# Optimization experiments

Measured on AMD Instinct MI355X. Metric: run time of the kernel, lower is better.

The kernel has to match this reference:

```python
import jax, jax.numpy as jnp
import numpy as np

H_OUT = 8
W_OUT = 8
MAXG = 4  # max adaptive sampling grid per bin: ceil((H-1)/H_OUT) with H=32


def _flip_table():
    h, w = H_OUT, W_OUT
    ys = np.repeat(np.arange(h), w)
    xs = np.tile(np.arange(w), h)
    rys = np.repeat(np.arange(h - 1, -1, -1), w)
    # NOTE: original torch code does arange(w-1,-1,-1).reshape(h,1).repeat(1,w)
    # which makes reverse_xs a per-ROW reversal (requires h==w); replicated faithfully.
    rxs = np.repeat(np.arange(w - 1, -1, -1), w)
    i00 = ys * w + xs
    i01 = ys * w + rxs
    i10 = rys * w + xs
    i11 = rys * w + rxs
    # original stacks [i00, i01, i01, i10, i11]; idx_idxs in {0..3} so entry for
    # (y_rev=1,x_rev=0) is i01 (duplicated) and (1,1) hits i10; i11 is unused. Replicated.
    return jnp.asarray(np.stack([i00, i01, i01, i10, i11]), dtype=jnp.int32)

_TABLE = _flip_table()


def _axis_samples(start, bin_sz, grid, n_out, size):
    # start, bin_sz: [N] float; grid: [N] int (adaptive samples per bin along this axis)
    # returns low/high neighbor indices and corner weights, each [N, n_out*MAXG]
    N = start.shape[0]
    g_safe = jnp.maximum(grid, 1).astype(start.dtype)
    ph = jnp.arange(n_out, dtype=start.dtype)
    i = jnp.arange(MAXG, dtype=start.dtype)
    pos = (start[:, None, None]
           + ph[None, :, None] * bin_sz[:, None, None]
           + (i[None, None, :] + 0.5) * (bin_sz / g_safe)[:, None, None])  # [N,n_out,MAXG]
    valid = ((pos >= -1.0) & (pos <= size)
             & (jnp.arange(MAXG)[None, None, :] < grid[:, None, None]))
    p = jnp.clip(pos, 0.0, size - 1)
    low = jnp.floor(p).astype(jnp.int32)
    high = jnp.minimum(low + 1, size - 1)
    l = p - low.astype(p.dtype)
    vf = valid.astype(start.dtype)
    return (low.reshape(N, -1), high.reshape(N, -1),
            ((1.0 - l) * vf).reshape(N, -1), (l * vf).reshape(N, -1))


def _roi_align_flip(feats, batch_idxs, starts, goals):
    B, C, H, W = feats.shape
    N = starts.shape[0]
    s = starts.astype(feats.dtype)
    g = goals.astype(feats.dtype)
    y_min = jnp.minimum(s[:, 0], g[:, 0]); y_max = jnp.maximum(s[:, 0], g[:, 0])
    x_min = jnp.minimum(s[:, 1], g[:, 1]); x_max = jnp.maximum(s[:, 1], g[:, 1])
    y_rev = s[:, 0] > g[:, 0]
    x_rev = s[:, 1] > g[:, 1]
    # torchvision roi_align: aligned=True, spatial_scale=1.0, sampling_ratio=-1
    start_h = y_min - 0.5; start_w = x_min - 0.5
    roi_h = y_max - y_min; roi_w = x_max - x_min
    bin_h = roi_h / H_OUT; bin_w = roi_w / W_OUT
    gh = jnp.ceil(bin_h).astype(jnp.int32)
    gw = jnp.ceil(bin_w).astype(jnp.int32)
    count = jnp.maximum(gh * gw, 1).astype(feats.dtype)
    ylo, yhi, wy0, wy1 = _axis_samples(start_h, bin_h, gh, H_OUT, H)  # [N, H_OUT*MAXG]
    xlo, xhi, wx0, wx1 = _axis_samples(start_w, bin_w, gw, W_OUT, W)  # [N, W_OUT*MAXG]
    fv = feats.reshape(B, C, H * W)[batch_idxs]  # [N,C,H*W] per-box feature slab
    hM, wM = H_OUT * MAXG, W_OUT * MAXG

    def gath(yi, xi):
        lin = (yi[:, :, None] * W + xi[:, None, :]).reshape(N, 1, hM * wM)
        v = jnp.take_along_axis(fv, jnp.broadcast_to(lin, (N, C, hM * wM)), axis=2)
        return v.reshape(N, C, hM, wM)

    def outer(a, b):
        return a[:, None, :, None] * b[:, None, None, :]

    acc = (gath(ylo, xlo) * outer(wy0, wx0)
           + gath(ylo, xhi) * outer(wy0, wx1)
           + gath(yhi, xlo) * outer(wy1, wx0)
           + gath(yhi, xhi) * outer(wy1, wx1))  # [N,C,hM,wM]
    rois = acc.reshape(N, C, H_OUT, MAXG, W_OUT, MAXG).sum(axis=(3, 5))
    rois = rois / count[:, None, None, None]
    # per-box orientation flip via index-table gather
    idx_idxs = y_rev.astype(jnp.int32) * 2 + x_rev.astype(jnp.int32)
    sel = _TABLE[idx_idxs]  # [N, h*w]
    rflat = rois.reshape(N, C, H_OUT * W_OUT)
    out = jnp.take_along_axis(rflat, jnp.broadcast_to(sel[:, None, :], rflat.shape), axis=2)
    return out.reshape(N, C, H_OUT, W_OUT)


def setup_inputs() -> dict:
    key = jax.random.key(0)
    k1, k2, k3, k4 = jax.random.split(key, 4)
    B, C, H, W = 8, 64, 32, 32
    N = 1024  # B * A with A = 128 agents
    feats = jax.random.normal(k1, (B, C, H, W), dtype=jnp.float32)
    batch_idxs = jax.random.randint(k2, (N,), 0, B, dtype=jnp.int32)
    starts = jax.random.randint(k3, (N, 2), 0, H, dtype=jnp.int32)
    goals = jax.random.randint(k4, (N, 2), 0, H, dtype=jnp.int32)
    return {"feats": feats, "batch_idxs": batch_idxs, "starts": starts, "goals": goals}


def reference(feats, batch_idxs, starts, goals):
    return _roi_align_flip(feats, batch_idxs, starts, goals)
```

## Files before the change

kernel.cpp:

```cpp
#include <hip/hip_runtime.h>

#define H_OUT 8
#define W_OUT 8
#define MAXG 4
#define CCHUNK 16
#define RSLOTS 6
#define TSTRIDE 160

__global__ __launch_bounds__(256) void build_tables(
    const int* __restrict__ batch_idxs,
    const int* __restrict__ starts,
    const int* __restrict__ goals,
    float*     __restrict__ tab, int N)
{
    const int t = blockIdx.x * 256 + threadIdx.x;
    if (t >= N * 16) return;
    const int n    = t >> 4;
    const int slot = t & 15;
    const int axis = slot >> 3;
    const int ph   = slot & 7;

    const float s0 = (float)starts[2 * n + 0];
    const float s1 = (float)starts[2 * n + 1];
    const float g0 = (float)goals[2 * n + 0];
    const float g1 = (float)goals[2 * n + 1];
    const float y_min = fminf(s0, g0), y_max = fmaxf(s0, g0);
    const float x_min = fminf(s1, g1), x_max = fmaxf(s1, g1);
    const float bin_h = (y_max - y_min) * 0.125f;
    const float bin_w = (x_max - x_min) * 0.125f;
    const int   gh = (int)ceilf(bin_h);
    const int   gw = (int)ceilf(bin_w);

    const float start = axis ? (x_min - 0.5f) : (y_min - 0.5f);
    const float bin   = axis ? bin_w : bin_h;
    const int   grid  = axis ? gw : gh;
    const float gsafe = (float)(grid > 1 ? grid : 1);

    float wloc[RSLOTS] = {0.f, 0.f, 0.f, 0.f, 0.f, 0.f};
    int base = 0, last = -1;
    for (int i = 0; i < grid; ++i) {
        const float pos = start + (float)ph * bin + ((float)i + 0.5f) * (bin / gsafe);
        const float vf  = (pos >= -1.0f && pos <= 32.0f) ? 1.0f : 0.0f;
        const float p   = fminf(fmaxf(pos, 0.0f), 31.0f);
        const int   lo  = (int)floorf(p);
        const int   hi  = min(lo + 1, 31);
        const float l   = p - (float)lo;
        if (i == 0) base = lo;
        wloc[lo - base] += (1.0f - l) * vf;
        wloc[hi - base] += l * vf;
        last = hi;
    }

    float* __restrict__ rec = tab + (size_t)n * TSTRIDE + axis * 64 + ph * 8;
    #pragma unroll
    for (int k = 0; k < RSLOTS; ++k) rec[k] = wloc[k];
    rec[6] = (float)base;
    rec[7] = (float)((grid > 0) ? (last - base + 1) : 0);
    if (slot == 0) {
        float* __restrict__ tb = tab + (size_t)n * TSTRIDE;
        const bool y_rev = s0 > g0;
        const bool x_rev = s1 > g1;
        tb[128] = 1.0f / fmaxf((float)(gh * gw), 1.0f);
        tb[129] = (float)((y_rev ? 2 : 0) + (x_rev ? 1 : 0));
        tb[130] = (float)batch_idxs[n];
        tb[131] = 0.0f;
    }
}

__global__ __launch_bounds__(256) void roi_main(
    const float* __restrict__ feats,
    const float* __restrict__ tab,
    float*       __restrict__ out,
    int C, int CG)
{
    const int bx  = blockIdx.x;
    const int n   = bx / CG;
    const int cg  = bx - n * CG;
    const int tid = threadIdx.x;

    const float* __restrict__ tb = tab + (size_t)n * TSTRIDE;

    __shared__ float s_t[CCHUNK][H_OUT][36];

    const int py = tid >> 5;
    const int cp = (tid >> 3) & 3;
    const int xq = tid & 7;
    const float4 ya   = *reinterpret_cast<const float4*>(tb + py * 8);
    const float4 yb   = *reinterpret_cast<const float4*>(tb + py * 8 + 4);
    const float4 meta = *reinterpret_cast<const float4*>(tb + 128);

    {
        const int rb = (int)yb.z;
        const int rc = (int)yb.w;
        const int b  = (int)meta.z;
        const float wy[6] = {ya.x, ya.y, ya.z, ya.w, yb.x, yb.y};

        const float* __restrict__ fb =
            feats + ((size_t)b * C + (size_t)(cg * CCHUNK + cp * 4)) * 1024 + xq * 4;

        float4 a0 = {0.f,0.f,0.f,0.f}, a1 = {0.f,0.f,0.f,0.f};
        float4 a2 = {0.f,0.f,0.f,0.f}, a3 = {0.f,0.f,0.f,0.f};
        #pragma unroll
        for (int j = 0; j < 5; ++j) {
            if (j < rc) {
                const float w  = wy[j];
                const int   ro = (rb + j) * 32;
                const float4 r0 = *reinterpret_cast<const float4*>(fb + ro);
                const float4 r1 = *reinterpret_cast<const float4*>(fb + 1024 + ro);
                const float4 r2 = *reinterpret_cast<const float4*>(fb + 2048 + ro);
                const float4 r3 = *reinterpret_cast<const float4*>(fb + 3072 + ro);
                a0.x = fmaf(w, r0.x, a0.x); a0.y = fmaf(w, r0.y, a0.y);
                a0.z = fmaf(w, r0.z, a0.z); a0.w = fmaf(w, r0.w, a0.w);
                a1.x = fmaf(w, r1.x, a1.x); a1.y = fmaf(w, r1.y, a1.y);
                a1.z = fmaf(w, r1.z, a1.z); a1.w = fmaf(w, r1.w, a1.w);
                a2.x = fmaf(w, r2.x, a2.x); a2.y = fmaf(w, r2.y, a2.y);
                a2.z = fmaf(w, r2.z, a2.z); a2.w = fmaf(w, r2.w, a2.w);
                a3.x = fmaf(w, r3.x, a3.x); a3.y = fmaf(w, r3.y, a3.y);
                a3.z = fmaf(w, r3.z, a3.z); a3.w = fmaf(w, r3.w, a3.w);
            }
        }
        const int x0 = xq * 4;
        *reinterpret_cast<float4*>(&s_t[cp * 4 + 0][py][x0]) = a0;
        *reinterpret_cast<float4*>(&s_t[cp * 4 + 1][py][x0]) = a1;
        *reinterpret_cast<float4*>(&s_t[cp * 4 + 2][py][x0]) = a2;
        *reinterpret_cast<float4*>(&s_t[cp * 4 + 3][py][x0]) = a3;
    }

    const int yx = tid & 63;
    const int y  = yx >> 3;
    const int xo = yx & 7;
    const int c0 = tid >> 6;

    const int fc = (int)meta.y;
    int py2, px;
    if (fc == 3)      { py2 = H_OUT - 1 - y; px = xo; }
    else if (fc != 0) { py2 = y;             px = W_OUT - 1 - y; }
    else              { py2 = y;             px = xo; }

    const float4 xa  = *reinterpret_cast<const float4*>(tb + 64 + px * 8);
    const float4 xb4 = *reinterpret_cast<const float4*>(tb + 64 + px * 8 + 4);

    __syncthreads();

    const int   xbi = (int)xb4.z;
    const int   xc  = (int)xb4.w;
    const float wx[6] = {xa.x, xa.y, xa.z, xa.w, xb4.x, xb4.y};
    const float inv_count = meta.x;

    float b0 = 0.f, b1 = 0.f, b2 = 0.f, b3 = 0.f;
    #pragma unroll
    for (int j = 0; j < 5; ++j) {
        if (j < xc) {
            const float w = wx[j];
            b0 = fmaf(w, s_t[c0     ][py2][xbi + j], b0);
            b1 = fmaf(w, s_t[c0 +  4][py2][xbi + j], b1);
            b2 = fmaf(w, s_t[c0 +  8][py2][xbi + j], b2);
            b3 = fmaf(w, s_t[c0 + 12][py2][xbi + j], b3);
        }
    }

    float* __restrict__ ob =
        out + ((size_t)n * C + (size_t)cg * CCHUNK) * (H_OUT * W_OUT);
    ob[tid      ] = b0 * inv_count;
    ob[tid + 256] = b1 * inv_count;
    ob[tid + 512] = b2 * inv_count;
    ob[tid + 768] = b3 * inv_count;
}

extern "C" void kernel_launch(void* const* d_in, const int* in_sizes, int n_in,
                              void* d_out, int out_size, void* d_ws, size_t ws_size,
                              hipStream_t stream) {
    const float* feats      = (const float*)d_in[0];
    const int*   batch_idxs = (const int*)d_in[1];
    const int*   starts     = (const int*)d_in[2];
    const int*   goals      = (const int*)d_in[3];
    float*       out        = (float*)d_out;
    float*       tab        = (float*)d_ws;

    const int N  = in_sizes[1];
    const int C  = out_size / (N * H_OUT * W_OUT);
    const int CG = C / CCHUNK;

    const int tb_blocks = (N * 16 + 255) / 256;
    build_tables<<<tb_blocks, 256, 0, stream>>>(batch_idxs, starts, goals, tab, N);
    roi_main<<<N * CG, 256, 0, stream>>>(feats, tab, out, C, CG);
}
```

Measured before the change: 76.63 us.

## Fuse per-box weight-table construction into main ROI kernel via shared memory

Removes the separate build_tables launch and the global workspace table. Each block now computes the per-box interpolation weights for both axes, plus the flip code and batch index, in its first 16 threads, stores them in shared memory, and synchronises before the main gather. This saves one kernel launch and a global round-trip, at the cost of redundant table computation in every channel-group block, a serial prologue executed by 16 threads, and an extra barrier.

```diff
diff --git a/kernel.cpp b/kernel.cpp
--- a/kernel.cpp
+++ b/kernel.cpp
@@ -2,74 +2,13 @@
 
 #define H_OUT 8
 #define W_OUT 8
-#define MAXG 4
 #define CCHUNK 16
-#define RSLOTS 6
-#define TSTRIDE 160
 
-__global__ __launch_bounds__(256) void build_tables(
-    const int* __restrict__ batch_idxs,
-    const int* __restrict__ starts,
-    const int* __restrict__ goals,
-    float*     __restrict__ tab, int N)
-{
-    const int t = blockIdx.x * 256 + threadIdx.x;
-    if (t >= N * 16) return;
-    const int n    = t >> 4;
-    const int slot = t & 15;
-    const int axis = slot >> 3;
-    const int ph   = slot & 7;
-
-    const float s0 = (float)starts[2 * n + 0];
-    const float s1 = (float)starts[2 * n + 1];
-    const float g0 = (float)goals[2 * n + 0];
-    const float g1 = (float)goals[2 * n + 1];
-    const float y_min = fminf(s0, g0), y_max = fmaxf(s0, g0);
-    const float x_min = fminf(s1, g1), x_max = fmaxf(s1, g1);
-    const float bin_h = (y_max - y_min) * 0.125f;
-    const float bin_w = (x_max - x_min) * 0.125f;
-    const int   gh = (int)ceilf(bin_h);
-    const int   gw = (int)ceilf(bin_w);
-
-    const float start = axis ? (x_min - 0.5f) : (y_min - 0.5f);
-    const float bin   = axis ? bin_w : bin_h;
-    const int   grid  = axis ? gw : gh;
-    const float gsafe = (float)(grid > 1 ? grid : 1);
-
-    float wloc[RSLOTS] = {0.f, 0.f, 0.f, 0.f, 0.f, 0.f};
-    int base = 0, last = -1;
-    for (int i = 0; i < grid; ++i) {
-        const float pos = start + (float)ph * bin + ((float)i + 0.5f) * (bin / gsafe);
-        const float vf  = (pos >= -1.0f && pos <= 32.0f) ? 1.0f : 0.0f;
-        const float p   = fminf(fmaxf(pos, 0.0f), 31.0f);
-        const int   lo  = (int)floorf(p);
-        const int   hi  = min(lo + 1, 31);
-        const float l   = p - (float)lo;
-        if (i == 0) base = lo;
-        wloc[lo - base] += (1.0f - l) * vf;
-        wloc[hi - base] += l * vf;
-        last = hi;
-    }
-
-    float* __restrict__ rec = tab + (size_t)n * TSTRIDE + axis * 64 + ph * 8;
-    #pragma unroll
-    for (int k = 0; k < RSLOTS; ++k) rec[k] = wloc[k];
-    rec[6] = (float)base;
-    rec[7] = (float)((grid > 0) ? (last - base + 1) : 0);
-    if (slot == 0) {
-        float* __restrict__ tb = tab + (size_t)n * TSTRIDE;
-        const bool y_rev = s0 > g0;
-        const bool x_rev = s1 > g1;
-        tb[128] = 1.0f / fmaxf((float)(gh * gw), 1.0f);
-        tb[129] = (float)((y_rev ? 2 : 0) + (x_rev ? 1 : 0));
-        tb[130] = (float)batch_idxs[n];
-        tb[131] = 0.0f;
-    }
-}
-
-__global__ __launch_bounds__(256) void roi_main(
+__global__ __launch_bounds__(256) void roi_fused(
     const float* __restrict__ feats,
-    const float* __restrict__ tab,
+    const int*   __restrict__ batch_idxs,
+    const int*   __restrict__ starts,
+    const int*   __restrict__ goals,
     float*       __restrict__ out,
     int C, int CG)
 {
@@ -78,22 +17,68 @@
     const int cg  = bx - n * CG;
     const int tid = threadIdx.x;
 
-    const float* __restrict__ tb = tab + (size_t)n * TSTRIDE;
+    __shared__ float s_rec[2][8][8];
+    __shared__ float s_meta[4];
+    __shared__ float s_t[CCHUNK][H_OUT][36];
 
-    __shared__ float s_t[CCHUNK][H_OUT][36];
+    if (tid < 16) {
+        const int axis = tid >> 3;
+        const int ph   = tid & 7;
+        const float s0 = (float)starts[2 * n + 0];
+        const float s1 = (float)starts[2 * n + 1];
+        const float g0 = (float)goals[2 * n + 0];
+        const float g1 = (float)goals[2 * n + 1];
+        const float y_min = fminf(s0, g0), y_max = fmaxf(s0, g0);
+        const float x_min = fminf(s1, g1), x_max = fmaxf(s1, g1);
+        const float bin_h = (y_max - y_min) * 0.125f;
+        const float bin_w = (x_max - x_min) * 0.125f;
+        const int   gh = (int)ceilf(bin_h);
+        const int   gw = (int)ceilf(bin_w);
+
+        const float start = axis ? (x_min - 0.5f) : (y_min - 0.5f);
+        const float bin   = axis ? bin_w : bin_h;
+        const int   grid  = axis ? gw : gh;
+        const float gsafe = (float)(grid > 1 ? grid : 1);
+
+        float* __restrict__ rec = &s_rec[axis][ph][0];
+        #pragma unroll
+        for (int k = 0; k < 6; ++k) rec[k] = 0.0f;
+
+        int base = 0, last = -1;
+        for (int i = 0; i < grid; ++i) {
+            const float pos = start + (float)ph * bin + ((float)i + 0.5f) * (bin / gsafe);
+            const float vf  = (pos >= -1.0f && pos <= 32.0f) ? 1.0f : 0.0f;
+            const float p   = fminf(fmaxf(pos, 0.0f), 31.0f);
+            const int   lo  = (int)floorf(p);
+            const int   hi  = min(lo + 1, 31);
+            const float l   = p - (float)lo;
+            if (i == 0) base = lo;
+            rec[lo - base] += (1.0f - l) * vf;
+            rec[hi - base] += l * vf;
+            last = hi;
+        }
+        rec[6] = (float)base;
+        rec[7] = (float)((grid > 0) ? (last - base + 1) : 0);
+        if (tid == 0) {
+            s_meta[0] = 1.0f / fmaxf((float)(gh * gw), 1.0f);
+            s_meta[1] = (float)(((s0 > g0) ? 2 : 0) + ((s1 > g1) ? 1 : 0));
+            s_meta[2] = (float)batch_idxs[n];
+        }
+    }
+    __syncthreads();
 
     const int py = tid >> 5;
     const int cp = (tid >> 3) & 3;
     const int xq = tid & 7;
-    const float4 ya   = *reinterpret_cast<const float4*>(tb + py * 8);
-    const float4 yb   = *reinterpret_cast<const float4*>(tb + py * 8 + 4);
-    const float4 meta = *reinterpret_cast<const float4*>(tb + 128);
-
+    const float4 ya = *reinterpret_cast<const float4*>(&s_rec[0][py][0]);
+    const float4 yb = *reinterpret_cast<const float4*>(&s_rec[0][py][4]);
+    const float inv_count = s_meta[0];
+    const int   fcode     = (int)s_meta[1];
+    const int   b         = (int)s_meta[2];
     {
         const int rb = (int)yb.z;
         const int rc = (int)yb.w;
-        const int b  = (int)meta.z;
-        const float wy[6] = {ya.x, ya.y, ya.z, ya.w, yb.x, yb.y};
+        const float wy[5] = {ya.x, ya.y, ya.z, ya.w, yb.x};
 
         const float* __restrict__ fb =
             feats + ((size_t)b * C + (size_t)(cg * CCHUNK + cp * 4)) * 1024 + xq * 4;
@@ -131,21 +116,19 @@
     const int xo = yx & 7;
     const int c0 = tid >> 6;
 
-    const int fc = (int)meta.y;
     int py2, px;
-    if (fc == 3)      { py2 = H_OUT - 1 - y; px = xo; }
-    else if (fc != 0) { py2 = y;             px = W_OUT - 1 - y; }
-    else              { py2 = y;             px = xo; }
+    if (fcode == 3)      { py2 = H_OUT - 1 - y; px = xo; }
+    else if (fcode != 0) { py2 = y;             px = W_OUT - 1 - y; }
+    else                 { py2 = y;             px = xo; }
 
-    const float4 xa  = *reinterpret_cast<const float4*>(tb + 64 + px * 8);
-    const float4 xb4 = *reinterpret_cast<const float4*>(tb + 64 + px * 8 + 4);
+    const float4 xa  = *reinterpret_cast<const float4*>(&s_rec[1][px][0]);
+    const float4 xb4 = *reinterpret_cast<const float4*>(&s_rec[1][px][4]);
 
     __syncthreads();
 
     const int   xbi = (int)xb4.z;
     const int   xc  = (int)xb4.w;
-    const float wx[6] = {xa.x, xa.y, xa.z, xa.w, xb4.x, xb4.y};
-    const float inv_count = meta.x;
+    const float wx[5] = {xa.x, xa.y, xa.z, xa.w, xb4.x};
 
     float b0 = 0.f, b1 = 0.f, b2 = 0.f, b3 = 0.f;
     #pragma unroll
@@ -175,13 +158,11 @@
     const int*   starts     = (const int*)d_in[2];
     const int*   goals      = (const int*)d_in[3];
     float*       out        = (float*)d_out;
-    float*       tab        = (float*)d_ws;
 
     const int N  = in_sizes[1];
     const int C  = out_size / (N * H_OUT * W_OUT);
     const int CG = C / CCHUNK;
 
-    const int tb_blocks = (N * 16 + 255) / 256;
-    build_tables<<<tb_blocks, 256, 0, stream>>>(batch_idxs, starts, goals, tab, N);
-    roi_main<<<N * CG, 256, 0, stream>>>(feats, tab, out, C, CG);
+    roi_fused<<<N * CG, 256, 0, stream>>>(feats, batch_idxs, starts, goals,
+                                          out, C, CG);
 }
```

Result: faster. 73.25 us (-4.4%).
